# Kernel optimization log

Hardware: AMD Instinct MI355X
Metric: run time of the kernel (lower is better)

Reference implementation:

```python
import jax, jax.numpy as jnp
import numpy as np

N_NODES = 50000
N_EDGES = 800000
D_IN = 768
D_H = 256
N_CLASSES = 4
N_LAYERS = 3
N_GRAPHS = 64
LN_EPS = 1e-5


def setup_inputs() -> dict:
    key = jax.random.key(0)
    ks = jax.random.split(key, 12)
    x = jax.random.normal(ks[0], (N_NODES, D_IN), dtype=jnp.float32)
    edge_index = jax.random.randint(ks[1], (2, N_EDGES), 0, N_NODES)
    batch = jnp.sort(jax.random.randint(ks[2], (N_NODES,), 0, N_GRAPHS))
    s_in = 1.0 / np.sqrt(D_IN)
    s_h = 1.0 / np.sqrt(D_H)
    W_in = jax.random.normal(ks[3], (D_IN, D_H), jnp.float32) * s_in
    b_in = jnp.zeros((D_H,), jnp.float32)
    convW = jax.random.normal(ks[4], (N_LAYERS, D_H, D_H), jnp.float32) * s_h
    convB = jnp.zeros((N_LAYERS, D_H), jnp.float32)
    lnG = jnp.ones((N_LAYERS, D_H), jnp.float32)
    lnB = jnp.zeros((N_LAYERS, D_H), jnp.float32)
    clsW1 = jax.random.normal(ks[5], (D_H, D_H), jnp.float32) * s_h
    clsB1 = jnp.zeros((D_H,), jnp.float32)
    clsW2 = jax.random.normal(ks[6], (D_H, N_CLASSES), jnp.float32) * s_h
    clsB2 = jnp.zeros((N_CLASSES,), jnp.float32)
    return {"x": x, "edge_index": edge_index, "batch": batch,
            "W_in": W_in, "b_in": b_in, "convW": convW, "convB": convB,
            "lnG": lnG, "lnB": lnB, "clsW1": clsW1, "clsB1": clsB1,
            "clsW2": clsW2, "clsB2": clsB2}


def _layer_norm(h, g, b):
    mu = jnp.mean(h, axis=-1, keepdims=True)
    var = jnp.mean(jnp.square(h - mu), axis=-1, keepdims=True)
    return (h - mu) * jax.lax.rsqrt(var + LN_EPS) * g + b


def reference(x, edge_index, batch, W_in, b_in, convW, convB, lnG, lnB,
              clsW1, clsB1, clsW2, clsB2):
    N = x.shape[0]
    loops = jnp.arange(N)
    src = jnp.concatenate([edge_index[0], loops])  # self-loops (PyG GCNConv default)
    dst = jnp.concatenate([edge_index[1], loops])
    deg = jax.ops.segment_sum(jnp.ones_like(src, dtype=x.dtype), dst, num_segments=N)
    dinv = jax.lax.rsqrt(deg)  # deg >= 1 due to self-loops
    norm = dinv[src] * dinv[dst]  # symmetric GCN normalization per edge

    h = x @ W_in + b_in  # input projection -> [N, D_H]
    for i in range(N_LAYERS):
        m = h @ convW[i]  # transform then propagate
        h_new = jax.ops.segment_sum(m[src] * norm[:, None], dst, num_segments=N) + convB[i]
        h = jax.nn.relu(h_new + h)  # residual (shapes match), then ReLU
        h = _layer_norm(h, lnG[i], lnB[i])
        # dropout: identity (inference mode)

    g = jax.ops.segment_max(h, batch, num_segments=N_GRAPHS)  # global_max_pool
    z = jax.nn.relu(g @ clsW1 + clsB1)
    return z @ clsW2 + clsB2  # [N_GRAPHS, N_CLASSES]
```

## Files before the change

### kernel.cpp

```cpp
#include <hip/hip_runtime.h>
#include <hip/hip_bf16.h>
#include <math.h>

#define NNODES 50000
#define NEDGES 800000
#define DIN 768
#define DH 256
#define NCLS 4
#define NGRAPHS 64
#define SCAN_BLOCKS 196
#define WSCHUNK 32
#define NCHUNKS ((NNODES + WSCHUNK - 1) / WSCHUNK)

typedef __bf16 bf16x8 __attribute__((ext_vector_type(8)));
typedef float f32x4 __attribute__((ext_vector_type(4)));

static __device__ __forceinline__ float bf2f(unsigned short u) {
    union { unsigned u32; float f; } v; v.u32 = ((unsigned)u) << 16; return v.f;
}
static __device__ __forceinline__ unsigned short f2bf(float f) {
    union { float f; unsigned u; } v; v.f = f;
    unsigned r = (v.u + 0x7fffu + ((v.u >> 16) & 1u)) >> 16;
    return (unsigned short)r;
}
static __device__ __forceinline__ void unpack8(uint4 u, float* f) {
    f[0] = bf2f((unsigned short)(u.x & 0xffff)); f[1] = bf2f((unsigned short)(u.x >> 16));
    f[2] = bf2f((unsigned short)(u.y & 0xffff)); f[3] = bf2f((unsigned short)(u.y >> 16));
    f[4] = bf2f((unsigned short)(u.z & 0xffff)); f[5] = bf2f((unsigned short)(u.z >> 16));
    f[6] = bf2f((unsigned short)(u.w & 0xffff)); f[7] = bf2f((unsigned short)(u.w >> 16));
}
static __device__ __forceinline__ void acc8(uint4 u, float* f) {
    f[0] += bf2f((unsigned short)(u.x & 0xffff)); f[1] += bf2f((unsigned short)(u.x >> 16));
    f[2] += bf2f((unsigned short)(u.y & 0xffff)); f[3] += bf2f((unsigned short)(u.y >> 16));
    f[4] += bf2f((unsigned short)(u.z & 0xffff)); f[5] += bf2f((unsigned short)(u.z >> 16));
    f[6] += bf2f((unsigned short)(u.w & 0xffff)); f[7] += bf2f((unsigned short)(u.w >> 16));
}
static __device__ __forceinline__ void gload_lds16(const void* g, void* l) {
    __builtin_amdgcn_global_load_lds((const __attribute__((address_space(1))) void*)g,
                                     (__attribute__((address_space(3))) void*)l, 16, 0, 0);
}

__global__ void detect_dtype(const unsigned short* __restrict__ x, int* __restrict__ flag) {
    __shared__ int cnt_s;
    if (threadIdx.x == 0) cnt_s = 0;
    __syncthreads();
    int c = 0;
    for (int i = 0; i < 16; ++i) {
        float v = bf2f(x[threadIdx.x * 16 + i]);
        if (!(fabsf(v) < 1e10f)) c++;
    }
    atomicAdd(&cnt_s, c);
    __syncthreads();
    if (threadIdx.x == 0) flag[0] = (cnt_s > 32) ? 1 : 0;
}

static __device__ __forceinline__ unsigned short cload(const void* src, int i, int fp32) {
    return fp32 ? f2bf(((const float*)src)[i]) : ((const unsigned short*)src)[i];
}

__global__ void canon_small(const void* b_in, const void* convB, const void* lnG,
                            const void* lnB, const void* W1, const void* W2,
                            const void* b1, const void* b2,
                            unsigned short* __restrict__ dst, const int* __restrict__ flag) {
    int i = blockIdx.x * 256 + threadIdx.x;
    if (i >= 69380) return;
    const int fp32 = flag[0];
    int j = i;
    if (j < 256)  { dst[i] = cload(b_in, j, fp32); return; }  j -= 256;
    if (j < 768)  { dst[i] = cload(convB, j, fp32); return; } j -= 768;
    if (j < 768)  { dst[i] = cload(lnG, j, fp32); return; }   j -= 768;
    if (j < 768)  { dst[i] = cload(lnB, j, fp32); return; }   j -= 768;
    if (j < 65536){ dst[i] = cload(W1, j, fp32); return; }    j -= 65536;
    if (j < 1024) { dst[i] = cload(W2, j, fp32); return; }    j -= 1024;
    if (j < 256)  { dst[i] = cload(b1, j, fp32); return; }    j -= 256;
    dst[i] = cload(b2, j, fp32);
}

__global__ void transpose_win(const void* __restrict__ src, unsigned short* __restrict__ dst,
                              const int* __restrict__ flag) {
    int idx = blockIdx.x * 256 + threadIdx.x;
    if (idx < DIN * DH) {
        int r = idx / DH, c = idx % DH;
        dst[(size_t)c * DIN + r] = cload(src, idx, flag[0]);
    }
}
__global__ void transpose_convw(const void* __restrict__ src, unsigned short* __restrict__ dst,
                                const int* __restrict__ flag) {
    int idx = blockIdx.x * 256 + threadIdx.x;
    if (idx < 3 * DH * DH) {
        int l = idx >> 16, rc = idx & 65535;
        int r = rc >> 8, c = rc & 255;
        dst[(l << 16) + c * DH + r] = cload(src, idx, flag[0]);
    }
}

__global__ void fill_sentinel(float* out, int n) {
    int i = blockIdx.x * 256 + threadIdx.x;
    if (i < n) out[i] = 1000.0f;
}

__global__ void count_edges(const int* __restrict__ ei, int* __restrict__ cnt) {
    int e = blockIdx.x * 256 + threadIdx.x;
    if (e < NEDGES) atomicAdd(&cnt[ei[NEDGES + e]], 1);
}

__global__ void scan_local(const int* __restrict__ cnt, int* __restrict__ rowptr,
                           int* __restrict__ bsum) {
    __shared__ int tmp[256];
    int i = blockIdx.x * 256 + threadIdx.x;
    int v = (i < NNODES) ? cnt[i] : 0;
    tmp[threadIdx.x] = v;
    __syncthreads();
    for (int off = 1; off < 256; off <<= 1) {
        int a = (threadIdx.x >= off) ? tmp[threadIdx.x - off] : 0;
        __syncthreads();
        tmp[threadIdx.x] += a;
        __syncthreads();
    }
    if (i < NNODES) rowptr[i] = tmp[threadIdx.x] - v;
    if (threadIdx.x == 255) bsum[blockIdx.x] = tmp[255];
}
__global__ void scan_bsum(const int* __restrict__ bsum, int* __restrict__ boff) {
    __shared__ int tmp[256];
    int t = threadIdx.x;
    int v = (t < SCAN_BLOCKS) ? bsum[t] : 0;
    tmp[t] = v;
    __syncthreads();
    for (int off = 1; off < 256; off <<= 1) {
        int a = (t >= off) ? tmp[t - off] : 0;
        __syncthreads();
        tmp[t] += a;
        __syncthreads();
    }
    if (t < SCAN_BLOCKS) boff[t] = tmp[t] - v;
}
__global__ void scan_finish(int* __restrict__ rowptr, const int* __restrict__ boff,
                            const int* __restrict__ cnt, float* __restrict__ dinv) {
    int i = blockIdx.x * 256 + threadIdx.x;
    if (i < NNODES) {
        rowptr[i] += boff[blockIdx.x];
        dinv[i] = rsqrtf((float)(1 + cnt[i]));
    }
    if (i == 0) rowptr[NNODES] = NEDGES;
}

__global__ void fill_csr(const int* __restrict__ ei, const int* __restrict__ rowptr,
                         int* __restrict__ cursor, int* __restrict__ csrc) {
    int e = blockIdx.x * 256 + threadIdx.x;
    if (e < NEDGES) {
        int s = ei[e];
        int d = ei[NEDGES + e];
        int pos = rowptr[d] + atomicAdd(&cursor[d], 1);
        csrc[pos] = s;
    }
}

__global__ __launch_bounds__(256, 3) void gemm_in(
    const void* __restrict__ Araw, const int* __restrict__ dflag,
    const unsigned short* __restrict__ Bt, const unsigned short* __restrict__ bias,
    unsigned short* __restrict__ C, int M, int K)
{
    __shared__ __align__(16) char As[2][8192];
    __shared__ __align__(16) char Bs[2][16384];

    const int af32 = dflag[0];
    const int m0 = blockIdx.x * 64;
    const int t = threadIdx.x, wave = t >> 6, lane = t & 63;
    const int quad = lane >> 4, l16 = lane & 15;

    const char* bsrc[4];
#pragma unroll
    for (int li = 0; li < 4; ++li) {
        int c = wave * 256 + li * 64 + lane;
        int r = c >> 2, p = c & 3;
        int l = p ^ ((r >> 1) & 3);
        bsrc[li] = (const char*)Bt + ((size_t)r * K + l * 8) * 2;
    }
    const char* asrc[2];
    if (af32) {
#pragma unroll
        for (int li = 0; li < 2; ++li) {
            int c = wave * 128 + li * 64 + lane;
            int r = c >> 3, p = c & 7;
            int l = p ^ (r & 7);
            int rg = min(m0 + r, M - 1);
            asrc[li] = (const char*)Araw + ((size_t)rg * K + l * 4) * 4;
        }
    } else {
        int c = wave * 64 + lane;
        int r = c >> 2, p = c & 3;
        int l = p ^ ((r >> 1) & 3);
        int rg = min(m0 + r, M - 1);
        asrc[0] = (const char*)Araw + ((size_t)rg * K + l * 8) * 2;
        asrc[1] = asrc[0];
    }

    f32x4 acc[4][4];
#pragma unroll
    for (int i = 0; i < 4; i++)
#pragma unroll
        for (int j = 0; j < 4; j++) acc[i][j] = (f32x4){0.f, 0.f, 0.f, 0.f};

    {
#pragma unroll
        for (int li = 0; li < 4; ++li)
            gload_lds16(bsrc[li], &Bs[0][(wave * 256 + li * 64) * 16]);
        if (af32) {
            gload_lds16(asrc[0], &As[0][(wave * 128) * 16]);
            gload_lds16(asrc[1], &As[0][(wave * 128 + 64) * 16]);
        } else {
            gload_lds16(asrc[0], &As[0][(wave * 64) * 16]);
        }
    }
    __syncthreads();

    const int nt = K / 32;
    for (int tt = 0; tt < nt; ++tt) {
        const int buf = tt & 1;
        if (tt + 1 < nt) {
            const size_t k0 = (size_t)(tt + 1) * 32;
#pragma unroll
            for (int li = 0; li < 4; ++li)
                gload_lds16(bsrc[li] + k0 * 2, &Bs[buf ^ 1][(wave * 256 + li * 64) * 16]);
            if (af32) {
                gload_lds16(asrc[0] + k0 * 4, &As[buf ^ 1][(wave * 128) * 16]);
                gload_lds16(asrc[1] + k0 * 4, &As[buf ^ 1][(wave * 128 + 64) * 16]);
            } else {
                gload_lds16(asrc[0] + k0 * 2, &As[buf ^ 1][(wave * 64) * 16]);
            }
        }
        const char* as_ = As[buf];
        const char* bs_ = Bs[buf];
        bf16x8 afv[4], bfv[4];
        if (af32) {
#pragma unroll
            for (int i = 0; i < 4; i++) {
                const int row = 16 * i + l16;
                const int ph0 = (quad * 2) ^ (row & 7);
                float4 x0 = *(const float4*)(as_ + row * 128 + ph0 * 16);
                float4 x1 = *(const float4*)(as_ + row * 128 + (ph0 ^ 1) * 16);
                union { bf16x8 v; __bf16 e[8]; } u;
                u.e[0] = (__bf16)x0.x; u.e[1] = (__bf16)x0.y;
                u.e[2] = (__bf16)x0.z; u.e[3] = (__bf16)x0.w;
                u.e[4] = (__bf16)x1.x; u.e[5] = (__bf16)x1.y;
                u.e[6] = (__bf16)x1.z; u.e[7] = (__bf16)x1.w;
                afv[i] = u.v;
            }
        } else {
            const int ph = (quad ^ ((l16 >> 1) & 3)) * 16;
#pragma unroll
            for (int i = 0; i < 4; i++)
                afv[i] = *(const bf16x8*)(as_ + (16 * i + l16) * 64 + ph);
        }
        {
            const int ph = (quad ^ ((l16 >> 1) & 3)) * 16;
#pragma unroll
            for (int j = 0; j < 4; j++)
                bfv[j] = *(const bf16x8*)(bs_ + (wave * 64 + 16 * j + l16) * 64 + ph);
        }
#pragma unroll
        for (int i = 0; i < 4; i++)
#pragma unroll
            for (int j = 0; j < 4; j++)
                acc[i][j] = __builtin_amdgcn_mfma_f32_16x16x32_bf16(afv[i], bfv[j], acc[i][j], 0, 0, 0);
        __syncthreads();
    }

#pragma unroll
    for (int j = 0; j < 4; j++) {
        const int gc = wave * 64 + 16 * j + l16;
        const float bv = bf2f(bias[gc]);
#pragma unroll
        for (int i = 0; i < 4; i++) {
#pragma unroll
            for (int rr = 0; rr < 4; rr++) {
                int gr = m0 + 16 * i + quad * 4 + rr;
                if (gr < M) C[(size_t)gr * 256 + gc] = f2bf(acc[i][j][rr] + bv);
            }
        }
    }
}

__global__ __launch_bounds__(512, 1) void gemm_ws(
    const unsigned short* __restrict__ A,
    const unsigned short* __restrict__ Bt,
    const float* __restrict__ prescale,
    unsigned short* __restrict__ C, int M)
{
    __shared__ __align__(16) unsigned short Bs[256 * 256];
    __shared__ __align__(16) unsigned short As[WSCHUNK * 256];

    const int t = threadIdx.x;
    const int wave = t >> 6, lane = t & 63;
    const int quad = lane >> 4, l16 = lane & 15;
    const int rf = wave & 1;
    const int cg = wave >> 1;

    for (int it = 0; it < 16; ++it) {
        int id = it * 512 + t;
        int col = id >> 5, p = id & 31;
        int l = p ^ (col & 31);
        gload_lds16(Bt + col * 256 + l * 8, (char*)Bs + id * 16);
    }
    {
        const int rbs = blockIdx.x * WSCHUNK;
#pragma unroll
        for (int it = 0; it < 2; ++it) {
            int id = it * 512 + t;
            int row = id >> 5, p = id & 31;
            int l = p ^ (row & 31);
            int rg = min(rbs + row, M - 1);
            gload_lds16(A + (size_t)rg * 256 + l * 8, (char*)As + id * 16);
        }
    }
    __syncthreads();

    for (int c = blockIdx.x; c < NCHUNKS; c += 256) {
        f32x4 acc[4];
#pragma unroll
        for (int j = 0; j < 4; ++j) acc[j] = (f32x4){0.f, 0.f, 0.f, 0.f};

        const int arow = rf * 16 + l16;
#pragma unroll
        for (int ks = 0; ks < 8; ++ks) {
            const int s = ks * 4 + quad;
            bf16x8 af = *(const bf16x8*)((const char*)As + arow * 512 + ((s ^ (arow & 31)) * 16));
#pragma unroll
            for (int j = 0; j < 4; ++j) {
                const int col = cg * 64 + j * 16 + l16;
                bf16x8 bf = *(const bf16x8*)((const char*)Bs + col * 512 + ((s ^ (col & 31)) * 16));
                acc[j] = __builtin_amdgcn_mfma_f32_16x16x32_bf16(af, bf, acc[j], 0, 0, 0);
            }
        }
        __syncthreads();

        const int cn = c + 256;
        if (cn < NCHUNKS) {
            const int rbs = cn * WSCHUNK;
#pragma unroll
            for (int it = 0; it < 2; ++it) {
                int id = it * 512 + t;
                int row = id >> 5, p = id & 31;
                int l = p ^ (row & 31);
                int rg = min(rbs + row, M - 1);
                gload_lds16(A + (size_t)rg * 256 + l * 8, (char*)As + id * 16);
            }
        }
        const int rb = c * WSCHUNK;
#pragma unroll
        for (int r = 0; r < 4; ++r) {
            const int gr = rb + rf * 16 + quad * 4 + r;
            if (gr < M) {
                const float sc = prescale[gr];
#pragma unroll
                for (int j = 0; j < 4; ++j) {
                    const int gc = cg * 64 + j * 16 + l16;
                    C[(size_t)gr * 256 + gc] = f2bf(acc[j][r] * sc);
                }
            }
        }
        __syncthreads();
    }
}

__global__ __launch_bounds__(256) void aggregate_ln(
    const int* __restrict__ rowptr, const int* __restrict__ csrc,
    const float* __restrict__ dinv, const unsigned short* __restrict__ m,
    const unsigned short* __restrict__ convB,
    const unsigned short* __restrict__ lnG, const unsigned short* __restrict__ lnB,
    unsigned short* __restrict__ h)
{
    const int half = threadIdx.x >> 5;
    const int lane = threadIdx.x & 31;
    const int node = blockIdx.x * 8 + half;
    const float di = dinv[node];
    const size_t base = (size_t)node * DH + lane * 8;
    const size_t lo = lane * 8;

    float v0[8], v1[8];
    unpack8(*(const uint4*)(m + base), v0);
#pragma unroll
    for (int j = 0; j < 8; j++) v1[j] = 0.f;

    const int kb = rowptr[node], ke = rowptr[node + 1];
    int k = kb;
    for (; k + 8 <= ke; k += 8) {
        int s0 = csrc[k],     s1 = csrc[k + 1], s2 = csrc[k + 2], s3 = csrc[k + 3];
        int s4 = csrc[k + 4], s5 = csrc[k + 5], s6 = csrc[k + 6], s7 = csrc[k + 7];
        uint4 r0 = *(const uint4*)(m + (size_t)s0 * DH + lo);
        uint4 r1 = *(const uint4*)(m + (size_t)s1 * DH + lo);
        uint4 r2 = *(const uint4*)(m + (size_t)s2 * DH + lo);
        uint4 r3 = *(const uint4*)(m + (size_t)s3 * DH + lo);
        uint4 r4 = *(const uint4*)(m + (size_t)s4 * DH + lo);
        uint4 r5 = *(const uint4*)(m + (size_t)s5 * DH + lo);
        uint4 r6 = *(const uint4*)(m + (size_t)s6 * DH + lo);
        uint4 r7 = *(const uint4*)(m + (size_t)s7 * DH + lo);
        acc8(r0, v0); acc8(r1, v1); acc8(r2, v0); acc8(r3, v1);
        acc8(r4, v0); acc8(r5, v1); acc8(r6, v0); acc8(r7, v1);
    }
    for (; k + 2 <= ke; k += 2) {
        int s0 = csrc[k], s1 = csrc[k + 1];
        uint4 r0 = *(const uint4*)(m + (size_t)s0 * DH + lo);
        uint4 r1 = *(const uint4*)(m + (size_t)s1 * DH + lo);
        acc8(r0, v0); acc8(r1, v1);
    }
    if (k < ke) {
        uint4 r0 = *(const uint4*)(m + (size_t)csrc[k] * DH + lo);
        acc8(r0, v0);
    }
#pragma unroll
    for (int j = 0; j < 8; j++) v0[j] = (v0[j] + v1[j]) * di;

    float hv[8], cv[8];
    unpack8(*(const uint4*)(h + base), hv);
    unpack8(*(const uint4*)(convB + lo), cv);
    float s1 = 0.f, s2 = 0.f;
#pragma unroll
    for (int j = 0; j < 8; j++) {
        v0[j] = fmaxf(v0[j] + cv[j] + hv[j], 0.f);
        s1 += v0[j];
        s2 += v0[j] * v0[j];
    }
#pragma unroll
    for (int off = 16; off > 0; off >>= 1) {
        s1 += __shfl_xor(s1, off, 32);
        s2 += __shfl_xor(s2, off, 32);
    }
    const float mu = s1 * (1.f / 256.f);
    const float var = s2 * (1.f / 256.f) - mu * mu;
    const float rs = rsqrtf(var + 1e-5f);
    float gv[8], bv[8];
    unpack8(*(const uint4*)(lnG + lo), gv);
    unpack8(*(const uint4*)(lnB + lo), bv);
    unsigned short o[8];
#pragma unroll
    for (int j = 0; j < 8; j++) o[j] = f2bf((v0[j] - mu) * rs * gv[j] + bv[j]);
    uint4 outp;
    outp.x = (unsigned)o[0] | ((unsigned)o[1] << 16);
    outp.y = (unsigned)o[2] | ((unsigned)o[3] << 16);
    outp.z = (unsigned)o[4] | ((unsigned)o[5] << 16);
    outp.w = (unsigned)o[6] | ((unsigned)o[7] << 16);
    *(uint4*)(h + base) = outp;
}

__global__ void find_bounds(const int* __restrict__ batch, int* __restrict__ s) {
    int i = blockIdx.x * 256 + threadIdx.x;
    if (i >= NNODES) return;
    int b = batch[i];
    int bp = (i == 0) ? -1 : batch[i - 1];
    for (int g = bp + 1; g <= b; ++g) s[g] = i;
    if (i == NNODES - 1)
        for (int g = b + 1; g <= NGRAPHS; ++g) s[g] = NNODES;
}

#define PSPLIT 8
__global__ __launch_bounds__(256) void pool_partial(
    const unsigned short* __restrict__ h, const int* __restrict__ s,
    float* __restrict__ pg)
{
    const int b = blockIdx.x >> 3, split = blockIdx.x & 7, f = threadIdx.x;
    const int i0 = s[b], i1 = s[b + 1];
    const int len = i1 - i0;
    const int c0 = i0 + (int)(((long)len * split) >> 3);
    const int c1 = i0 + (int)(((long)len * (split + 1)) >> 3);
    float mx = -INFINITY;
    for (int i = c0; i < c1; ++i) mx = fmaxf(mx, bf2f(h[(size_t)i * DH + f]));
    pg[(size_t)blockIdx.x * DH + f] = mx;
}
__global__ __launch_bounds__(256) void pool_reduce(const float* __restrict__ pg,
                                                   float* __restrict__ g) {
    const int b = blockIdx.x, f = threadIdx.x;
    float mx = -INFINITY;
#pragma unroll
    for (int j = 0; j < PSPLIT; ++j) mx = fmaxf(mx, pg[(size_t)(b * PSPLIT + j) * DH + f]);
    g[b * DH + f] = mx;
}

__global__ __launch_bounds__(256) void classifier(
    const float* __restrict__ g, const unsigned short* __restrict__ W1,
    const unsigned short* __restrict__ b1, const unsigned short* __restrict__ W2,
    const unsigned short* __restrict__ b2, void* __restrict__ outv,
    const int* __restrict__ flag)
{
    __shared__ float gz[DH];
    __shared__ float zz[DH];
    const int b = blockIdx.x, t = threadIdx.x;
    gz[t] = g[b * DH + t];
    __syncthreads();
    float s = bf2f(b1[t]);
    for (int k = 0; k < DH; ++k) s += gz[k] * bf2f(W1[k * DH + t]);
    zz[t] = fmaxf(s, 0.f);
    __syncthreads();
    if (t < NCLS) {
        float s2 = bf2f(b2[t]);
        for (int k = 0; k < DH; ++k) s2 += zz[k] * bf2f(W2[k * NCLS + t]);
        if (flag[0]) ((float*)outv)[b * NCLS + t] = s2;
        else ((unsigned short*)outv)[b * NCLS + t] = f2bf(s2);
    }
}

extern "C" void kernel_launch(void* const* d_in, const int* in_sizes, int n_in,
                              void* d_out, int out_size, void* d_ws, size_t ws_size,
                              hipStream_t stream)
{
    const void* x      = d_in[0];
    const int* ei      = (const int*)d_in[1];
    const int* batch   = (const int*)d_in[2];
    const void* Win    = d_in[3];
    const void* b_in   = d_in[4];
    const void* convW  = d_in[5];
    const void* convB  = d_in[6];
    const void* lnG    = d_in[7];
    const void* lnB    = d_in[8];
    const void* W1     = d_in[9];
    const void* b1     = d_in[10];
    const void* W2     = d_in[11];
    const void* b2     = d_in[12];

    char* ws = (char*)d_ws;
    unsigned short* h   = (unsigned short*)(ws + 0);
    unsigned short* m   = (unsigned short*)(ws + 25600000);
    int* csrc           = (int*)(ws + 51200000);
    int* rowptr         = (int*)(ws + 54400000);
    int* cnt            = (int*)(ws + 54600016);
    int* cursor         = (int*)(ws + 54800016);
    float* dinv         = (float*)(ws + 55000016);
    unsigned short* cw  = (unsigned short*)(ws + 55200016);
    unsigned short* WinT= (unsigned short*)(ws + 55338784);
    unsigned short* WcT = (unsigned short*)(ws + 55732000);
    float* g            = (float*)(ws + 56125216);
    float* pg           = (float*)(ws + 56190752);
    int* gb             = (int*)(ws + 56715040);
    int* bsum           = (int*)(ws + 56715312);
    int* boff           = (int*)(ws + 56716112);
    int* flag           = (int*)(ws + 56716912);
    const size_t NEED   = 56716928;
    if (ws_size < NEED) {
        fill_sentinel<<<(out_size / 2 + 255) / 256, 256, 0, stream>>>((float*)d_out, out_size / 2);
        return;
    }

    unsigned short* cBin   = cw + 0;
    unsigned short* cConvB = cw + 256;
    unsigned short* cLnG   = cw + 1024;
    unsigned short* cLnB   = cw + 1792;
    unsigned short* cW1    = cw + 2560;
    unsigned short* cW2    = cw + 68096;
    unsigned short* cB1    = cw + 69120;
    unsigned short* cB2    = cw + 69376;

    detect_dtype<<<1, 256, 0, stream>>>((const unsigned short*)x, flag);

    hipMemsetAsync(cnt, 0, 400000, stream);
    count_edges<<<(NEDGES + 255) / 256, 256, 0, stream>>>(ei, cnt);
    scan_local<<<SCAN_BLOCKS, 256, 0, stream>>>(cnt, rowptr, bsum);
    scan_bsum<<<1, 256, 0, stream>>>(bsum, boff);
    scan_finish<<<SCAN_BLOCKS, 256, 0, stream>>>(rowptr, boff, cnt, dinv);
    fill_csr<<<(NEDGES + 255) / 256, 256, 0, stream>>>(ei, rowptr, cursor, csrc);

    canon_small<<<(69380 + 255) / 256, 256, 0, stream>>>(b_in, convB, lnG, lnB, W1, W2, b1, b2, cw, flag);
    transpose_win<<<(DIN * DH + 255) / 256, 256, 0, stream>>>(Win, WinT, flag);
    transpose_convw<<<(3 * DH * DH + 255) / 256, 256, 0, stream>>>(convW, WcT, flag);

    gemm_in<<<(NNODES + 63) / 64, 256, 0, stream>>>(x, flag, WinT, cBin, h, NNODES, DIN);

    for (int i = 0; i < 3; i++) {
        gemm_ws<<<256, 512, 0, stream>>>(h, WcT + i * DH * DH, dinv, m, NNODES);
        aggregate_ln<<<NNODES / 8, 256, 0, stream>>>(
            rowptr, csrc, dinv, m, cConvB + i * DH, cLnG + i * DH, cLnB + i * DH, h);
    }

    find_bounds<<<(NNODES + 255) / 256, 256, 0, stream>>>(batch, gb);
    pool_partial<<<NGRAPHS * PSPLIT, 256, 0, stream>>>(h, gb, pg);
    pool_reduce<<<NGRAPHS, 256, 0, stream>>>(pg, g);
    classifier<<<NGRAPHS, 256, 0, stream>>>(g, cW1, cB1, cW2, cB2, d_out, flag);
}
```

Baseline: 681.9 us.

## Triple-buffer gemm_in LDS tiles with partial vmcnt waits

```diff
diff --git a/kernel.cpp b/kernel.cpp
--- a/kernel.cpp
+++ b/kernel.cpp
@@ -155,13 +155,13 @@
     }
 }
 
-__global__ __launch_bounds__(256, 3) void gemm_in(
+__global__ __launch_bounds__(256, 2) void gemm_in(
     const void* __restrict__ Araw, const int* __restrict__ dflag,
     const unsigned short* __restrict__ Bt, const unsigned short* __restrict__ bias,
     unsigned short* __restrict__ C, int M, int K)
 {
-    __shared__ __align__(16) char As[2][8192];
-    __shared__ __align__(16) char Bs[2][16384];
+    __shared__ __align__(16) char As[3][8192];
+    __shared__ __align__(16) char Bs[3][16384];
 
     const int af32 = dflag[0];
     const int m0 = blockIdx.x * 64;
@@ -195,42 +195,41 @@
         asrc[1] = asrc[0];
     }
 
+    auto stage = [&](int tile, int bi) {
+        const size_t k0 = (size_t)tile * 32;
+#pragma unroll
+        for (int li = 0; li < 4; ++li)
+            gload_lds16(bsrc[li] + k0 * 2, &Bs[bi][(wave * 256 + li * 64) * 16]);
+        if (af32) {
+            gload_lds16(asrc[0] + k0 * 4, &As[bi][(wave * 128) * 16]);
+            gload_lds16(asrc[1] + k0 * 4, &As[bi][(wave * 128 + 64) * 16]);
+        } else {
+            gload_lds16(asrc[0] + k0 * 2, &As[bi][(wave * 64) * 16]);
+        }
+    };
+
     f32x4 acc[4][4];
 #pragma unroll
     for (int i = 0; i < 4; i++)
 #pragma unroll
         for (int j = 0; j < 4; j++) acc[i][j] = (f32x4){0.f, 0.f, 0.f, 0.f};
 
-    {
-#pragma unroll
-        for (int li = 0; li < 4; ++li)
-            gload_lds16(bsrc[li], &Bs[0][(wave * 256 + li * 64) * 16]);
-        if (af32) {
-            gload_lds16(asrc[0], &As[0][(wave * 128) * 16]);
-            gload_lds16(asrc[1], &As[0][(wave * 128 + 64) * 16]);
-        } else {
-            gload_lds16(asrc[0], &As[0][(wave * 64) * 16]);
-        }
-    }
-    __syncthreads();
+    stage(0, 0);
+    stage(1, 1);
+    if (af32) asm volatile("s_waitcnt vmcnt(6)" ::: "memory");
+    else      asm volatile("s_waitcnt vmcnt(5)" ::: "memory");
+    __builtin_amdgcn_sched_barrier(0);
+    __builtin_amdgcn_s_barrier();
+    __builtin_amdgcn_sched_barrier(0);
 
     const int nt = K / 32;
     for (int tt = 0; tt < nt; ++tt) {
-        const int buf = tt & 1;
-        if (tt + 1 < nt) {
-            const size_t k0 = (size_t)(tt + 1) * 32;
-#pragma unroll
-            for (int li = 0; li < 4; ++li)
-                gload_lds16(bsrc[li] + k0 * 2, &Bs[buf ^ 1][(wave * 256 + li * 64) * 16]);
-            if (af32) {
-                gload_lds16(asrc[0] + k0 * 4, &As[buf ^ 1][(wave * 128) * 16]);
-                gload_lds16(asrc[1] + k0 * 4, &As[buf ^ 1][(wave * 128 + 64) * 16]);
-            } else {
-                gload_lds16(asrc[0] + k0 * 2, &As[buf ^ 1][(wave * 64) * 16]);
-            }
-        }
-        const char* as_ = As[buf];
-        const char* bs_ = Bs[buf];
+        const int bi = tt % 3;
+        const bool deep = (tt + 2) < nt;
+        if (deep) stage(tt + 2, (tt + 2) % 3);
+
+        const char* as_ = As[bi];
+        const char* bs_ = Bs[bi];
         bf16x8 afv[4], bfv[4];
         if (af32) {
 #pragma unroll
@@ -263,7 +262,16 @@
 #pragma unroll
             for (int j = 0; j < 4; j++)
                 acc[i][j] = __builtin_amdgcn_mfma_f32_16x16x32_bf16(afv[i], bfv[j], acc[i][j], 0, 0, 0);
-        __syncthreads();
+
+        if (deep) {
+            if (af32) asm volatile("s_waitcnt vmcnt(6)" ::: "memory");
+            else      asm volatile("s_waitcnt vmcnt(5)" ::: "memory");
+        } else {
+            asm volatile("s_waitcnt vmcnt(0)" ::: "memory");
+        }
+        __builtin_amdgcn_sched_barrier(0);
+        __builtin_amdgcn_s_barrier();
+        __builtin_amdgcn_sched_barrier(0);
     }
 
 #pragma unroll
```

Measured after the change: 672.6 us. Within noise of the previous version (-1.4%).

## Preload full A row-tile as bf16 in gemm_in, vectorize pooling

Applied to the files above, without the earlier changes.

```diff
diff --git a/kernel.cpp b/kernel.cpp
--- a/kernel.cpp
+++ b/kernel.cpp
@@ -11,6 +11,8 @@
 #define SCAN_BLOCKS 196
 #define WSCHUNK 32
 #define NCHUNKS ((NNODES + WSCHUNK - 1) / WSCHUNK)
+#define IMB 32
+#define INBLK ((NNODES + IMB - 1) / IMB)
 
 typedef __bf16 bf16x8 __attribute__((ext_vector_type(8)));
 typedef float f32x4 __attribute__((ext_vector_type(4)));
@@ -155,16 +157,16 @@
     }
 }
 
-__global__ __launch_bounds__(256, 3) void gemm_in(
+__global__ __launch_bounds__(256, 2) void gemm_in(
     const void* __restrict__ Araw, const int* __restrict__ dflag,
     const unsigned short* __restrict__ Bt, const unsigned short* __restrict__ bias,
     unsigned short* __restrict__ C, int M, int K)
 {
-    __shared__ __align__(16) char As[2][8192];
+    __shared__ __align__(16) char As[IMB * 1536];
     __shared__ __align__(16) char Bs[2][16384];
 
     const int af32 = dflag[0];
-    const int m0 = blockIdx.x * 64;
+    const int m0 = blockIdx.x * IMB;
     const int t = threadIdx.x, wave = t >> 6, lane = t & 63;
     const int quad = lane >> 4, l16 = lane & 15;
 
@@ -176,43 +178,47 @@
         int l = p ^ ((r >> 1) & 3);
         bsrc[li] = (const char*)Bt + ((size_t)r * K + l * 8) * 2;
     }
-    const char* asrc[2];
+
+#pragma unroll
+    for (int li = 0; li < 4; ++li)
+        gload_lds16(bsrc[li], &Bs[0][(wave * 256 + li * 64) * 16]);
+
     if (af32) {
-#pragma unroll
-        for (int li = 0; li < 2; ++li) {
-            int c = wave * 128 + li * 64 + lane;
-            int r = c >> 3, p = c & 7;
-            int l = p ^ (r & 7);
-            int rg = min(m0 + r, M - 1);
-            asrc[li] = (const char*)Araw + ((size_t)rg * K + l * 4) * 4;
+        for (int it = 0; it < 12; ++it) {
+            int id = it * 256 + t;
+            int row = id / 96, c = id - row * 96;
+            int kt = c >> 2, sl = (c & 3) ^ (row & 3);
+            int rg = min(m0 + row, M - 1);
+            const float* src = (const float*)Araw + (size_t)rg * K + c * 8;
+            float4 f0 = *(const float4*)src;
+            float4 f1 = *(const float4*)(src + 4);
+            unsigned short o[8];
+            o[0] = f2bf(f0.x); o[1] = f2bf(f0.y); o[2] = f2bf(f0.z); o[3] = f2bf(f0.w);
+            o[4] = f2bf(f1.x); o[5] = f2bf(f1.y); o[6] = f2bf(f1.z); o[7] = f2bf(f1.w);
+            uint4 u;
+            u.x = (unsigned)o[0] | ((unsigned)o[1] << 16);
+            u.y = (unsigned)o[2] | ((unsigned)o[3] << 16);
+            u.z = (unsigned)o[4] | ((unsigned)o[5] << 16);
+            u.w = (unsigned)o[6] | ((unsigned)o[7] << 16);
+            *(uint4*)(&As[row * 1536 + kt * 64 + sl * 16]) = u;
         }
     } else {
-        int c = wave * 64 + lane;
-        int r = c >> 2, p = c & 3;
-        int l = p ^ ((r >> 1) & 3);
-        int rg = min(m0 + r, M - 1);
-        asrc[0] = (const char*)Araw + ((size_t)rg * K + l * 8) * 2;
-        asrc[1] = asrc[0];
-    }
-
-    f32x4 acc[4][4];
-#pragma unroll
-    for (int i = 0; i < 4; i++)
+        for (int it = 0; it < 12; ++it) {
+            int id = it * 256 + t;
+            int row = id / 96, c = id - row * 96;
+            int kt = c >> 2, sl = (c & 3) ^ (row & 3);
+            int rg = min(m0 + row, M - 1);
+            uint4 u = *(const uint4*)((const unsigned short*)Araw + (size_t)rg * K + c * 8);
+            *(uint4*)(&As[row * 1536 + kt * 64 + sl * 16]) = u;
+        }
+    }
+    __syncthreads();
+
+    f32x4 acc[2][4];
+#pragma unroll
+    for (int i = 0; i < 2; i++)
 #pragma unroll
         for (int j = 0; j < 4; j++) acc[i][j] = (f32x4){0.f, 0.f, 0.f, 0.f};
-
-    {
-#pragma unroll
-        for (int li = 0; li < 4; ++li)
-            gload_lds16(bsrc[li], &Bs[0][(wave * 256 + li * 64) * 16]);
-        if (af32) {
-            gload_lds16(asrc[0], &As[0][(wave * 128) * 16]);
-            gload_lds16(asrc[1], &As[0][(wave * 128 + 64) * 16]);
-        } else {
-            gload_lds16(asrc[0], &As[0][(wave * 64) * 16]);
-        }
-    }
-    __syncthreads();
 
     const int nt = K / 32;
     for (int tt = 0; tt < nt; ++tt) {
@@ -222,44 +228,22 @@
 #pragma unroll
             for (int li = 0; li < 4; ++li)
                 gload_lds16(bsrc[li] + k0 * 2, &Bs[buf ^ 1][(wave * 256 + li * 64) * 16]);
-            if (af32) {
-                gload_lds16(asrc[0] + k0 * 4, &As[buf ^ 1][(wave * 128) * 16]);
-                gload_lds16(asrc[1] + k0 * 4, &As[buf ^ 1][(wave * 128 + 64) * 16]);
-            } else {
-                gload_lds16(asrc[0] + k0 * 2, &As[buf ^ 1][(wave * 64) * 16]);
-            }
-        }
-        const char* as_ = As[buf];
-        const char* bs_ = Bs[buf];
-        bf16x8 afv[4], bfv[4];
-        if (af32) {
-#pragma unroll
-            for (int i = 0; i < 4; i++) {
-                const int row = 16 * i + l16;
-                const int ph0 = (quad * 2) ^ (row & 7);
-                float4 x0 = *(const float4*)(as_ + row * 128 + ph0 * 16);
-                float4 x1 = *(const float4*)(as_ + row * 128 + (ph0 ^ 1) * 16);
-                union { bf16x8 v; __bf16 e[8]; } u;
-                u.e[0] = (__bf16)x0.x; u.e[1] = (__bf16)x0.y;
-                u.e[2] = (__bf16)x0.z; u.e[3] = (__bf16)x0.w;
-                u.e[4] = (__bf16)x1.x; u.e[5] = (__bf16)x1.y;
-                u.e[6] = (__bf16)x1.z; u.e[7] = (__bf16)x1.w;
-                afv[i] = u.v;
-            }
-        } else {
-            const int ph = (quad ^ ((l16 >> 1) & 3)) * 16;
-#pragma unroll
-            for (int i = 0; i < 4; i++)
-                afv[i] = *(const bf16x8*)(as_ + (16 * i + l16) * 64 + ph);
+        }
+        bf16x8 afv[2], bfv[4];
+#pragma unroll
+        for (int i = 0; i < 2; i++) {
+            const int row = 16 * i + l16;
+            afv[i] = *(const bf16x8*)(&As[row * 1536 + tt * 64 + ((quad ^ (row & 3)) * 16)]);
         }
         {
             const int ph = (quad ^ ((l16 >> 1) & 3)) * 16;
+            const char* bs_ = Bs[buf];
 #pragma unroll
             for (int j = 0; j < 4; j++)
                 bfv[j] = *(const bf16x8*)(bs_ + (wave * 64 + 16 * j + l16) * 64 + ph);
         }
 #pragma unroll
-        for (int i = 0; i < 4; i++)
+        for (int i = 0; i < 2; i++)
 #pragma unroll
             for (int j = 0; j < 4; j++)
                 acc[i][j] = __builtin_amdgcn_mfma_f32_16x16x32_bf16(afv[i], bfv[j], acc[i][j], 0, 0, 0);
@@ -271,7 +255,7 @@
         const int gc = wave * 64 + 16 * j + l16;
         const float bv = bf2f(bias[gc]);
 #pragma unroll
-        for (int i = 0; i < 4; i++) {
+        for (int i = 0; i < 2; i++) {
 #pragma unroll
             for (int rr = 0; rr < 4; rr++) {
                 int gr = m0 + 16 * i + quad * 4 + rr;
@@ -458,14 +442,30 @@
     const unsigned short* __restrict__ h, const int* __restrict__ s,
     float* __restrict__ pg)
 {
-    const int b = blockIdx.x >> 3, split = blockIdx.x & 7, f = threadIdx.x;
+    __shared__ float red[8][DH];
+    const int b = blockIdx.x >> 3, split = blockIdx.x & 7;
+    const int g = threadIdx.x >> 5, lane = threadIdx.x & 31;
     const int i0 = s[b], i1 = s[b + 1];
     const int len = i1 - i0;
     const int c0 = i0 + (int)(((long)len * split) >> 3);
     const int c1 = i0 + (int)(((long)len * (split + 1)) >> 3);
-    float mx = -INFINITY;
-    for (int i = c0; i < c1; ++i) mx = fmaxf(mx, bf2f(h[(size_t)i * DH + f]));
-    pg[(size_t)blockIdx.x * DH + f] = mx;
+    float mx[8];
+#pragma unroll
+    for (int j = 0; j < 8; ++j) mx[j] = -INFINITY;
+    for (int r = c0 + g; r < c1; r += 8) {
+        uint4 v = *(const uint4*)(h + (size_t)r * DH + lane * 8);
+        float f[8];
+        unpack8(v, f);
+#pragma unroll
+        for (int j = 0; j < 8; ++j) mx[j] = fmaxf(mx[j], f[j]);
+    }
+#pragma unroll
+    for (int j = 0; j < 8; ++j) red[g][lane * 8 + j] = mx[j];
+    __syncthreads();
+    const int f = threadIdx.x;
+    float m0 = fmaxf(fmaxf(red[0][f], red[1][f]), fmaxf(red[2][f], red[3][f]));
+    float m1 = fmaxf(fmaxf(red[4][f], red[5][f]), fmaxf(red[6][f], red[7][f]));
+    pg[(size_t)blockIdx.x * DH + f] = fmaxf(m0, m1);
 }
 __global__ __launch_bounds__(256) void pool_reduce(const float* __restrict__ pg,
                                                    float* __restrict__ g) {
@@ -562,7 +562,7 @@
     transpose_win<<<(DIN * DH + 255) / 256, 256, 0, stream>>>(Win, WinT, flag);
     transpose_convw<<<(3 * DH * DH + 255) / 256, 256, 0, stream>>>(convW, WcT, flag);
 
-    gemm_in<<<(NNODES + 63) / 64, 256, 0, stream>>>(x, flag, WinT, cBin, h, NNODES, DIN);
+    gemm_in<<<INBLK, 256, 0, stream>>>(x, flag, WinT, cBin, h, NNODES, DIN);
 
     for (int i = 0; i < 3; i++) {
         gemm_ws<<<256, 512, 0, stream>>>(h, WcT + i * DH * DH, dinv, m, NNODES);
```

New measurement: 703.7 us. 1.03x slower.
